# Kernel tuning notes

Hardware: AMD Instinct MI355X
Metric: run time of the kernel (lower is better)

The kernel has to match this reference:

```python
import jax, jax.numpy as jnp
import numpy as np

N_LEVELS = 16
N_FEATS = 2
LOG2_T = 19
TABLE_SIZE = 2 ** LOG2_T
BASE_RES = 16
FINEST_RES = 2048
N_POINTS = 2_000_000

# growth factor b = (N_max/N_min)^(1/(L-1))
_B = np.exp((np.log(FINEST_RES) - np.log(BASE_RES)) / (N_LEVELS - 1))
# primes[1:4] from the torch module (pi_1 is multiplied into x, etc.)
_PRIMES = np.array([2654435761, 805459861, 3674653429], dtype=np.uint32)
# corner offsets in the same (dx, dy, dz) nesting order as the torch loops
_OFFSETS = np.array([[dx, dy, dz] for dx in (0, 1) for dy in (0, 1) for dz in (0, 1)], dtype=np.int32)


def setup_inputs() -> dict:
    key = jax.random.key(0)
    k1, k2 = jax.random.split(key)
    positions = jax.random.uniform(k1, (N_POINTS, 3), dtype=jnp.float32)  # in [0,1)
    # nn.init.uniform_(table.weight, -1e-4, 1e-4)
    hash_tables = jax.random.uniform(k2, (N_LEVELS, TABLE_SIZE, N_FEATS),
                                     dtype=jnp.float32, minval=-1e-4, maxval=1e-4)
    return {"positions": positions, "hash_tables": hash_tables}


def reference(positions, hash_tables):
    # positions: [N,3] float; hash_tables: [L,T,F] float
    primes = jnp.asarray(_PRIMES)            # uint32
    offsets = jnp.asarray(_OFFSETS)          # [8,3] int32
    off_is_one = (offsets == 1)[None]        # [1,8,3] bool
    feats = []
    for level in range(N_LEVELS):
        res = min(int(BASE_RES * _B ** level), FINEST_RES)
        scaled = positions * (res - 1)                       # [N,3]
        grid = jnp.floor(scaled).astype(jnp.int32)           # [N,3]
        w = scaled - grid.astype(scaled.dtype)               # [N,3] interp weights
        corners = jnp.clip(grid[:, None, :] + offsets[None], 0, res - 1)  # [N,8,3]
        # spatial hash: (x*p1 ^ y*p2 ^ z*p3) mod 2^19. Torch does this in int64;
        # because the modulus is a power of two (low 19 bits) and coords are
        # non-negative, uint32 wraparound arithmetic gives identical results.
        cu = corners.astype(jnp.uint32)
        h = ((cu[..., 0] * primes[0]) ^ (cu[..., 1] * primes[1]) ^ (cu[..., 2] * primes[2]))
        idx = (h % jnp.uint32(TABLE_SIZE)).astype(jnp.int32)  # [N,8]
        cf = hash_tables[level][idx]                          # [N,8,F] gather
        # trilinear corner weights: prod_d (w_d if off_d==1 else 1-w_d)
        cw = jnp.prod(jnp.where(off_is_one, w[:, None, :], 1.0 - w[:, None, :]), axis=-1)  # [N,8]
        feats.append(jnp.sum(cf * cw[..., None], axis=1))    # [N,F]
    return jnp.concatenate(feats, axis=-1)                   # [N, L*F]
```

## Files before the change

### kernel.cpp

```cpp
#include <hip/hip_runtime.h>
#include <hip/hip_fp16.h>
#include <math.h>


#define NLV 16
#define TSZ (1 << 19)
#define TMASK (TSZ - 1)
#define BLK 256
#define MAXDENSE 7
#define ROWH2 (NLV + 1)
#define ROWF 34

struct P16 {
    int r[NLV];
    int doff[MAXDENSE + 1];
    int ndense;
};

__device__ __forceinline__ float2 enc_level(
    const float px, const float py, const float pz,
    const int res, const float2* __restrict__ tl)
{
    const unsigned P1 = 2654435761u, P2 = 805459861u, P3 = 3674653429u;
    const float scale = (float)(res - 1);
    const float sx = px * scale, sy = py * scale, sz = pz * scale;
    const float fx = floorf(sx), fy = floorf(sy), fz = floorf(sz);
    const float wx = sx - fx, wy = sy - fy, wz = sz - fz;
    const int gx = (int)fx, gy = (int)fy, gz = (int)fz;
    const int rm = res - 1;
    const int x0 = min(max(gx, 0), rm), x1 = min(max(gx + 1, 0), rm);
    const int y0 = min(max(gy, 0), rm), y1 = min(max(gy + 1, 0), rm);
    const int z0 = min(max(gz, 0), rm), z1 = min(max(gz + 1, 0), rm);
    const unsigned hx0 = (unsigned)x0 * P1, hx1 = (unsigned)x1 * P1;
    const unsigned hy0 = (unsigned)y0 * P2, hy1 = (unsigned)y1 * P2;
    const unsigned hz0 = (unsigned)z0 * P3, hz1 = (unsigned)z1 * P3;

    const float2 c000 = tl[(hx0 ^ hy0 ^ hz0) & TMASK];
    const float2 c001 = tl[(hx0 ^ hy0 ^ hz1) & TMASK];
    const float2 c010 = tl[(hx0 ^ hy1 ^ hz0) & TMASK];
    const float2 c011 = tl[(hx0 ^ hy1 ^ hz1) & TMASK];
    const float2 c100 = tl[(hx1 ^ hy0 ^ hz0) & TMASK];
    const float2 c101 = tl[(hx1 ^ hy0 ^ hz1) & TMASK];
    const float2 c110 = tl[(hx1 ^ hy1 ^ hz0) & TMASK];
    const float2 c111 = tl[(hx1 ^ hy1 ^ hz1) & TMASK];

    const float ux = 1.f - wx, uy = 1.f - wy, uz = 1.f - wz;
    const float a00 = ux * uy, a01 = ux * wy, a10 = wx * uy, a11 = wx * wy;
    const float w000 = a00 * uz, w001 = a00 * wz;
    const float w010 = a01 * uz, w011 = a01 * wz;
    const float w100 = a10 * uz, w101 = a10 * wz;
    const float w110 = a11 * uz, w111 = a11 * wz;

    float acc0 = c000.x * w000;           float acc1 = c000.y * w000;
    acc0 += c001.x * w001;                acc1 += c001.y * w001;
    acc0 += c010.x * w010;                acc1 += c010.y * w010;
    acc0 += c011.x * w011;                acc1 += c011.y * w011;
    acc0 += c100.x * w100;                acc1 += c100.y * w100;
    acc0 += c101.x * w101;                acc1 += c101.y * w101;
    acc0 += c110.x * w110;                acc1 += c110.y * w110;
    acc0 += c111.x * w111;                acc1 += c111.y * w111;
    return make_float2(acc0, acc1);
}

__device__ __forceinline__ float2 enc_dense(
    const float px, const float py, const float pz,
    const int res, const float4* __restrict__ G)
{
    const float scale = (float)(res - 1);
    const float sx = px * scale, sy = py * scale, sz = pz * scale;
    int gx = (int)floorf(sx), gy = (int)floorf(sy), gz = (int)floorf(sz);
    gx = min(max(gx, 0), res - 2);
    gy = min(max(gy, 0), res - 2);
    gz = min(max(gz, 0), res - 2);
    const float wx = sx - (float)gx, wy = sy - (float)gy, wz = sz - (float)gz;

    const int r00 = (gz * res + gy) * res + gx;
    const int r10 = r00 + res;
    const int r01 = r00 + res * res;
    const int r11 = r01 + res;
    const float4 v00 = G[r00];
    const float4 v10 = G[r10];
    const float4 v01 = G[r01];
    const float4 v11 = G[r11];

    const float ux = 1.f - wx;
    const float uy = 1.f - wy, uz = 1.f - wz;
    const float b00 = uy * uz, b10 = wy * uz, b01 = uy * wz, b11 = wy * wz;
    float acc0 = (v00.x * ux + v00.z * wx) * b00;
    float acc1 = (v00.y * ux + v00.w * wx) * b00;
    acc0 += (v10.x * ux + v10.z * wx) * b10;
    acc1 += (v10.y * ux + v10.w * wx) * b10;
    acc0 += (v01.x * ux + v01.z * wx) * b01;
    acc1 += (v01.y * ux + v01.w * wx) * b01;
    acc0 += (v11.x * ux + v11.z * wx) * b11;
    acc1 += (v11.y * ux + v11.w * wx) * b11;
    return make_float2(acc0, acc1);
}

__global__ __launch_bounds__(BLK) void build_dense_kernel(
    const float* __restrict__ tab, float4* __restrict__ dg,
    const P16 pp, const int total)
{
    const unsigned P1 = 2654435761u, P2 = 805459861u, P3 = 3674653429u;
    const int i = blockIdx.x * BLK + threadIdx.x;
    if (i >= total) return;
    int l = 0;
    #pragma unroll
    for (int k = 1; k < MAXDENSE; ++k)
        if (k < pp.ndense && i >= pp.doff[k]) l = k;
    const int res = pp.r[l], rm = res - 1;
    const int id = i - pp.doff[l];
    const int x = id % res;
    const int t2 = id / res;
    const int y = t2 % res;
    const int z = t2 / res;
    const float2* T = ((const float2*)tab) + (long long)l * TSZ;
    const unsigned hyz = ((unsigned)y * P2) ^ ((unsigned)z * P3);
    const float2 lo = T[(((unsigned)x * P1) ^ hyz) & TMASK];
    const int x1 = min(x + 1, rm);
    const float2 hi = T[(((unsigned)x1 * P1) ^ hyz) & TMASK];
    dg[i] = make_float4(lo.x, lo.y, hi.x, hi.y);
}

__global__ __launch_bounds__(BLK) void pass1_kernel(
    const float* __restrict__ pos,
    const float* __restrict__ tab,
    __half2* __restrict__ wsh,
    const float4* __restrict__ dense,
    const P16 pp, const int npts, const int nblk_per_level)
{
    const int level = blockIdx.x / nblk_per_level;
    const int chunk = blockIdx.x % nblk_per_level;
    const long long n = (long long)chunk * BLK + threadIdx.x;
    if (n >= npts) return;

    const float px = pos[n * 3 + 0];
    const float py = pos[n * 3 + 1];
    const float pz = pos[n * 3 + 2];

    float2 f;
    if (level < pp.ndense) {
        f = enc_dense(px, py, pz, pp.r[level], dense + pp.doff[level]);
    } else {
        const float2* tl = ((const float2*)tab) + (long long)level * TSZ;
        f = enc_level(px, py, pz, pp.r[level], tl);
    }
    wsh[(long long)level * npts + n] = __float22half2_rn(f);
}

__global__ __launch_bounds__(BLK) void pass2_kernel(
    const __half2* __restrict__ wsh,
    float4* __restrict__ out4,
    const int npts)
{
    __shared__ __half2 l2s[BLK][ROWH2];
    const int t = threadIdx.x;
    const long long p0 = (long long)blockIdx.x * BLK;

    #pragma unroll
    for (int k = 0; k < 8; ++k) {
        const int idx = k * BLK + t;
        const int l = idx >> 7;
        const int j = idx & 127;
        const long long base = p0 + 2 * j;
        union { uint2 u; __half2 h[2]; } cv;
        cv.u = make_uint2(0u, 0u);
        const __half2* src = wsh + (long long)l * npts + p0;
        if (base + 1 < npts) {
            cv.u = ((const uint2*)src)[j];
        } else if (base < npts) {
            cv.h[0] = src[2 * j];
        }
        l2s[2 * j + 0][l] = cv.h[0];
        l2s[2 * j + 1][l] = cv.h[1];
    }
    __syncthreads();

    #pragma unroll
    for (int k = 0; k < 8; ++k) {
        const int idx = k * BLK + t;
        const int pt = idx >> 3;
        const int q = idx & 7;
        const long long np = p0 + pt;
        if (np < npts) {
            const float2 a = __half22float2(l2s[pt][2 * q + 0]);
            const float2 b = __half22float2(l2s[pt][2 * q + 1]);
            out4[np * 8 + q] = make_float4(a.x, a.y, b.x, b.y);
        }
    }
}

__global__ __launch_bounds__(BLK) void fused_kernel(
    const float* __restrict__ pos,
    const float* __restrict__ tab,
    float* __restrict__ out,
    const P16 pp, const int npts)
{
    __shared__ float lds[BLK * ROWF];
    const int t = threadIdx.x;
    const long long blk = blockIdx.x;
    const long long n = blk * BLK + t;

    float px = 0.f, py = 0.f, pz = 0.f;
    if (n < npts) {
        px = pos[n * 3 + 0];
        py = pos[n * 3 + 1];
        pz = pos[n * 3 + 2];
    }
    for (int l = 0; l < NLV; ++l) {
        const float2* tl = ((const float2*)tab) + (long long)l * TSZ;
        const float2 f = enc_level(px, py, pz, pp.r[l], tl);
        lds[t * ROWF + 2 * l + 0] = f.x;
        lds[t * ROWF + 2 * l + 1] = f.y;
    }
    __syncthreads();
    float2* o2 = (float2*)out;
    const float2* l2 = (const float2*)lds;
    const long long obase = blk * (BLK * 16);
    const long long lim = (long long)npts * 16;
    #pragma unroll
    for (int k = 0; k < 16; ++k) {
        const long long g = obase + (long long)k * BLK + t;
        if (g < lim) {
            const int lp = (int)((g >> 4) - blk * BLK);
            const int fp = (int)(g & 15);
            o2[g] = l2[lp * 17 + fp];
        }
    }
}

extern "C" void kernel_launch(void* const* d_in, const int* in_sizes, int n_in,
                              void* d_out, int out_size, void* d_ws, size_t ws_size,
                              hipStream_t stream) {
    const float* pos = (const float*)d_in[0];
    const float* tab = (const float*)d_in[1];
    float* out = (float*)d_out;
    const int npts = in_sizes[0] / 3;
    if (npts <= 0) return;

    P16 pp;
    const double B = exp((log(2048.0) - log(16.0)) / 15.0);
    for (int l = 0; l < NLV; ++l) {
        const double v = 16.0 * pow(B, (double)l);
        int r = (int)v;
        if (r > 2048) r = 2048;
        pp.r[l] = r;
    }

    const size_t ws_needed = (size_t)NLV * npts * sizeof(__half2);
    const int nblk = (npts + BLK - 1) / BLK;

    pp.ndense = 0;
    long long cum = 0;
    for (int l = 0; l < MAXDENSE; ++l) {
        const long long cells = (long long)pp.r[l] * pp.r[l] * pp.r[l];
        if (ws_needed + (size_t)(cum + cells) * sizeof(float4) <= ws_size) {
            pp.doff[l] = (int)cum;
            cum += cells;
            pp.ndense++;
        } else break;
    }
    for (int l = pp.ndense; l <= MAXDENSE; ++l) pp.doff[l] = (int)cum;

    if (ws_size >= ws_needed) {
        __half2* wsh = (__half2*)d_ws;
        float4* dense = (float4*)((char*)d_ws + ws_needed);
        if (pp.ndense > 0) {
            const int total = (int)cum;
            hipLaunchKernelGGL(build_dense_kernel, dim3((total + BLK - 1) / BLK), dim3(BLK),
                               0, stream, tab, dense, pp, total);
        }
        hipLaunchKernelGGL(pass1_kernel, dim3(nblk * NLV), dim3(BLK), 0, stream,
                           pos, tab, wsh, dense, pp, npts, nblk);
        hipLaunchKernelGGL(pass2_kernel, dim3(nblk), dim3(BLK), 0, stream,
                           wsh, (float4*)out, npts);
    } else {
        hipLaunchKernelGGL(fused_kernel, dim3(nblk), dim3(BLK), 0, stream,
                           pos, tab, out, pp, npts);
    }
}
```

Measured before the change: 1.305 ms.

## Pack 2x2 dense-grid cell corners as fp16 to halve dense gathers

```diff
diff --git a/kernel.cpp b/kernel.cpp
--- a/kernel.cpp
+++ b/kernel.cpp
@@ -16,6 +16,8 @@
     int doff[MAXDENSE + 1];
     int ndense;
 };
+
+union QuadCell { float4 f4; __half2 h[4]; };
 
 __device__ __forceinline__ float2 enc_level(
     const float px, const float py, const float pz,
@@ -74,27 +76,27 @@
     gz = min(max(gz, 0), res - 2);
     const float wx = sx - (float)gx, wy = sy - (float)gy, wz = sz - (float)gz;
 
-    const int r00 = (gz * res + gy) * res + gx;
-    const int r10 = r00 + res;
-    const int r01 = r00 + res * res;
-    const int r11 = r01 + res;
-    const float4 v00 = G[r00];
-    const float4 v10 = G[r10];
-    const float4 v01 = G[r01];
-    const float4 v11 = G[r11];
-
-    const float ux = 1.f - wx;
-    const float uy = 1.f - wy, uz = 1.f - wz;
-    const float b00 = uy * uz, b10 = wy * uz, b01 = uy * wz, b11 = wy * wz;
-    float acc0 = (v00.x * ux + v00.z * wx) * b00;
-    float acc1 = (v00.y * ux + v00.w * wx) * b00;
-    acc0 += (v10.x * ux + v10.z * wx) * b10;
-    acc1 += (v10.y * ux + v10.w * wx) * b10;
-    acc0 += (v01.x * ux + v01.z * wx) * b01;
-    acc1 += (v01.y * ux + v01.w * wx) * b01;
-    acc0 += (v11.x * ux + v11.z * wx) * b11;
-    acc1 += (v11.y * ux + v11.w * wx) * b11;
-    return make_float2(acc0, acc1);
+    const int r0 = (gz * res + gy) * res + gx;
+    const int r1 = r0 + res * res;
+    QuadCell q0, q1;
+    q0.f4 = G[r0];
+    q1.f4 = G[r1];
+
+    const float ux = 1.f - wx, uy = 1.f - wy, uz = 1.f - wz;
+    const float2 a00 = __half22float2(q0.h[0]);
+    const float2 a10 = __half22float2(q0.h[1]);
+    const float2 a01 = __half22float2(q0.h[2]);
+    const float2 a11 = __half22float2(q0.h[3]);
+    const float2 b00 = __half22float2(q1.h[0]);
+    const float2 b10 = __half22float2(q1.h[1]);
+    const float2 b01 = __half22float2(q1.h[2]);
+    const float2 b11 = __half22float2(q1.h[3]);
+
+    const float m0x = (a00.x * ux + a10.x * wx) * uy + (a01.x * ux + a11.x * wx) * wy;
+    const float m0y = (a00.y * ux + a10.y * wx) * uy + (a01.y * ux + a11.y * wx) * wy;
+    const float m1x = (b00.x * ux + b10.x * wx) * uy + (b01.x * ux + b11.x * wx) * wy;
+    const float m1y = (b00.y * ux + b10.y * wx) * uy + (b01.y * ux + b11.y * wx) * wy;
+    return make_float2(m0x * uz + m1x * wz, m0y * uz + m1y * wz);
 }
 
 __global__ __launch_bounds__(BLK) void build_dense_kernel(
@@ -115,11 +117,21 @@
     const int y = t2 % res;
     const int z = t2 / res;
     const float2* T = ((const float2*)tab) + (long long)l * TSZ;
-    const unsigned hyz = ((unsigned)y * P2) ^ ((unsigned)z * P3);
-    const float2 lo = T[(((unsigned)x * P1) ^ hyz) & TMASK];
     const int x1 = min(x + 1, rm);
-    const float2 hi = T[(((unsigned)x1 * P1) ^ hyz) & TMASK];
-    dg[i] = make_float4(lo.x, lo.y, hi.x, hi.y);
+    const int y1 = min(y + 1, rm);
+    const unsigned hx0 = (unsigned)x * P1, hx1 = (unsigned)x1 * P1;
+    const unsigned hy0 = (unsigned)y * P2, hy1 = (unsigned)y1 * P2;
+    const unsigned hz = (unsigned)z * P3;
+    const float2 c00 = T[(hx0 ^ hy0 ^ hz) & TMASK];
+    const float2 c10 = T[(hx1 ^ hy0 ^ hz) & TMASK];
+    const float2 c01 = T[(hx0 ^ hy1 ^ hz) & TMASK];
+    const float2 c11 = T[(hx1 ^ hy1 ^ hz) & TMASK];
+    QuadCell q;
+    q.h[0] = __float22half2_rn(c00);
+    q.h[1] = __float22half2_rn(c10);
+    q.h[2] = __float22half2_rn(c01);
+    q.h[3] = __float22half2_rn(c11);
+    dg[i] = q.f4;
 }
 
 __global__ __launch_bounds__(BLK) void pass1_kernel(
```

Result: faster. 1.161 ms (-11.0%).
